# Kernel optimization log

Measured on AMD Instinct MI355X. Metric: run time of the kernel, lower is better.

The kernel has to match this reference:

```python
import jax, jax.numpy as jnp
import numpy as np

N_NODES = 100000
N_EDGES = 1600000
IN_SIZE = 512
HID_SIZE = 256
OUT_SIZE = 40
K_STEPS = 10
ALPHA = 0.1


def setup_inputs() -> dict:
    key = jax.random.key(0)
    ks = jax.random.split(key, 8)
    features = jax.random.normal(ks[0], (N_NODES, IN_SIZE), dtype=jnp.float32)
    src = jax.random.randint(ks[1], (N_EDGES,), 0, N_NODES, dtype=jnp.int64)
    dst = jax.random.randint(ks[2], (N_EDGES,), 0, N_NODES, dtype=jnp.int64)
    # MLP params (Kaiming-ish scale)
    W1 = jax.random.normal(ks[3], (IN_SIZE, HID_SIZE), dtype=jnp.float32) / np.sqrt(IN_SIZE)
    b1 = jnp.zeros((HID_SIZE,), dtype=jnp.float32)
    W2 = jax.random.normal(ks[4], (HID_SIZE, OUT_SIZE), dtype=jnp.float32) / np.sqrt(HID_SIZE)
    b2 = jnp.zeros((OUT_SIZE,), dtype=jnp.float32)
    return {"features": features, "src": src, "dst": dst,
            "W1": W1, "b1": b1, "W2": W2, "b2": b2}


def reference(features, src, dst, W1, b1, W2, b2):
    # --- MLP encoder (dropout is identity in eval mode) ---
    h = jax.nn.relu(features @ W1 + b1)
    h = h @ W2 + b2  # [N, out_size]

    # --- Symmetric normalization (DGL APPNPConv, edge_weight=None) ---
    ones_e = jnp.ones((src.shape[0],), dtype=h.dtype)
    deg_out = jax.ops.segment_sum(ones_e, src, num_segments=N_NODES)
    deg_in = jax.ops.segment_sum(ones_e, dst, num_segments=N_NODES)
    norm_src = jnp.power(jnp.clip(deg_out, 1.0), -0.5)[:, None]  # D_out^{-1/2}
    norm_dst = jnp.power(jnp.clip(deg_in, 1.0), -0.5)[:, None]   # D_in^{-1/2}

    # --- k=10 APPNP propagation: h <- (1-a) * D^{-1/2} A D^{-1/2} h + a * h0 ---
    h0 = h

    def step(h, _):
        msg = (h * norm_src)[src]                                  # gather [E, out]
        agg = jax.ops.segment_sum(msg, dst, num_segments=N_NODES)  # scatter-add
        h = (1.0 - ALPHA) * (agg * norm_dst) + ALPHA * h0
        return h, None

    h, _ = jax.lax.scan(step, h, None, length=K_STEPS)
    return h
```

## Files before the change

kernel.cpp:

```cpp
#include <hip/hip_runtime.h>

#define N_NODES 100000
#define N_EDGES 1600000
#define IN_SIZE 512
#define HID_SIZE 256
#define OUT_SIZE 40
#define K_STEPS 10
#define ALPHA 0.1f

#define NCH 250
#define CH_E 6400
#define NBUK 391
#define NRS 8
#define HRS 12544
#define NCS 16
#define CS_E 100000

typedef _Float16 half8 __attribute__((ext_vector_type(8)));
typedef float f32x4 __attribute__((ext_vector_type(4)));

struct __align__(8) Entry { int s; int d; };

__global__ __launch_bounds__(512) void hist_pass(const int* __restrict__ dst,
                                                 int* __restrict__ cnt) {
    __shared__ int h[NBUK];
    const int t = threadIdx.x, c = blockIdx.x;
    for (int j = t; j < NBUK; j += 512) h[j] = 0;
    __syncthreads();
    const int4* d4 = (const int4*)(dst + c * CH_E);
    for (int i = t; i < CH_E / 4; i += 512) {
        const int4 v = d4[i];
        atomicAdd(&h[v.x >> 8], 1);
        atomicAdd(&h[v.y >> 8], 1);
        atomicAdd(&h[v.z >> 8], 1);
        atomicAdd(&h[v.w >> 8], 1);
    }
    __syncthreads();
    for (int j = t; j < NBUK; j += 512) cnt[c * NBUK + j] = h[j];
}

__global__ __launch_bounds__(512) void bucket_scan(const int* __restrict__ cnt,
                                                   int* __restrict__ off,
                                                   int* __restrict__ boff) {
    __shared__ int tot[512];
    const int b = threadIdx.x;
    int s = 0;
    if (b < NBUK)
        for (int c = 0; c < NCH; ++c) s += cnt[c * NBUK + b];
    tot[b] = s;
    __syncthreads();
    for (int o = 1; o < 512; o <<= 1) {
        const int v = (b >= o) ? tot[b - o] : 0;
        __syncthreads();
        tot[b] += v;
        __syncthreads();
    }
    if (b < NBUK) {
        int run = tot[b] - s;
        boff[b] = run;
        for (int c = 0; c < NCH; ++c) { off[c * NBUK + b] = run; run += cnt[c * NBUK + b]; }
        if (b == NBUK - 1) boff[NBUK] = tot[b];
    }
}

__global__ __launch_bounds__(512) void scatter_pass(const int* __restrict__ src,
                                                    const int* __restrict__ dst,
                                                    const int* __restrict__ off,
                                                    Entry* __restrict__ ebuf) {
    __shared__ int cur[NBUK];
    const int t = threadIdx.x, c = blockIdx.x;
    for (int j = t; j < NBUK; j += 512) cur[j] = off[c * NBUK + j];
    __syncthreads();
    const int4* s4 = (const int4*)(src + c * CH_E);
    const int4* d4 = (const int4*)(dst + c * CH_E);
    for (int i = t; i < CH_E / 4; i += 512) {
        const int4 sv = s4[i];
        const int4 dv = d4[i];
        Entry e;
        int p;
        p = atomicAdd(&cur[dv.x >> 8], 1); e.s = sv.x; e.d = dv.x; ebuf[p] = e;
        p = atomicAdd(&cur[dv.y >> 8], 1); e.s = sv.y; e.d = dv.y; ebuf[p] = e;
        p = atomicAdd(&cur[dv.z >> 8], 1); e.s = sv.z; e.d = dv.z; ebuf[p] = e;
        p = atomicAdd(&cur[dv.w >> 8], 1); e.s = sv.w; e.d = dv.w; ebuf[p] = e;
    }
}

__global__ __launch_bounds__(256) void bucket_csr(const Entry* __restrict__ ebuf,
                                                  const int* __restrict__ boff,
                                                  int* __restrict__ rowp,
                                                  float* __restrict__ ndst,
                                                  int* __restrict__ csr) {
    __shared__ int hist[256];
    __shared__ int pref[256];
    __shared__ int cur[256];
    const int t = threadIdx.x, b = blockIdx.x;
    const int beg = boff[b], end = boff[b + 1];
    hist[t] = 0;
    __syncthreads();
    for (int i = beg + t; i < end; i += 256)
        atomicAdd(&hist[ebuf[i].d & 255], 1);
    __syncthreads();
    const int h = hist[t];
    pref[t] = h;
    __syncthreads();
    for (int o = 1; o < 256; o <<= 1) {
        const int v = (t >= o) ? pref[t - o] : 0;
        __syncthreads();
        pref[t] += v;
        __syncthreads();
    }
    const int val = beg + pref[t] - h;
    const int n = (b << 8) + t;
    if (n <= N_NODES) rowp[n] = val;
    if (n < N_NODES) ndst[n] = 1.0f / sqrtf((float)max(h, 1));
    cur[t] = val;
    __syncthreads();
    for (int i = beg + t; i < end; i += 256) {
        const Entry e = ebuf[i];
        const int pos = atomicAdd(&cur[e.d & 255], 1);
        csr[pos] = e.s;
    }
}

__global__ __launch_bounds__(512) void degsrc_part(const int* __restrict__ src,
                                                   int* __restrict__ partial) {
    __shared__ int h[HRS];
    const int t = threadIdx.x;
    const int r = blockIdx.x & (NRS - 1);
    const int c = blockIdx.x >> 3;
    const int base = r * HRS;
    for (int j = t; j < HRS; j += 512) h[j] = 0;
    __syncthreads();
    const int4* s4 = (const int4*)(src + (size_t)c * CS_E);
    for (int i = t; i < CS_E / 4; i += 512) {
        const int4 v = s4[i];
        unsigned u;
        u = (unsigned)(v.x - base); if (u < HRS) atomicAdd(&h[u], 1);
        u = (unsigned)(v.y - base); if (u < HRS) atomicAdd(&h[u], 1);
        u = (unsigned)(v.z - base); if (u < HRS) atomicAdd(&h[u], 1);
        u = (unsigned)(v.w - base); if (u < HRS) atomicAdd(&h[u], 1);
    }
    __syncthreads();
    for (int j = t; j < HRS; j += 512) partial[(size_t)c * (NRS * HRS) + base + j] = h[j];
}

__global__ __launch_bounds__(256) void nsrc_reduce(const int* __restrict__ partial,
                                                   float* __restrict__ nsrc) {
    const int n = blockIdx.x * 256 + threadIdx.x;
    int s = 0;
#pragma unroll
    for (int c = 0; c < NCS; ++c) s += partial[(size_t)c * (NRS * HRS) + n];
    if (n < N_NODES) nsrc[n] = 1.0f / sqrtf((float)max(s, 1));
}

__global__ __launch_bounds__(256) void prep_w(const float* __restrict__ W1,
                                              const float* __restrict__ W2,
                                              unsigned short* __restrict__ w1t,
                                              unsigned short* __restrict__ w2t) {
    int idx = blockIdx.x * 256 + threadIdx.x;
    if (idx < IN_SIZE * HID_SIZE) {
        int n = idx >> 9;
        int k = idx & 511;
        _Float16 h = (_Float16)W1[(size_t)k * HID_SIZE + n];
        w1t[idx] = *(unsigned short*)&h;
    } else if (idx < IN_SIZE * HID_SIZE + 48 * HID_SIZE) {
        int i2 = idx - IN_SIZE * HID_SIZE;
        int o = i2 >> 8;
        int c = i2 & 255;
        float v = (o < OUT_SIZE) ? W2[(size_t)c * OUT_SIZE + o] : 0.f;
        _Float16 h = (_Float16)v;
        w2t[i2] = *(unsigned short*)&h;
    }
}

__global__ __launch_bounds__(512) void gemm_fused(const float* __restrict__ X,
                                                  const unsigned short* __restrict__ w1t,
                                                  const float* __restrict__ b1,
                                                  const unsigned short* __restrict__ w2t,
                                                  const float* __restrict__ b2,
                                                  const float* __restrict__ nsrc,
                                                  _Float16* __restrict__ h0a,
                                                  _Float16* __restrict__ g0) {
    __shared__ __align__(16) unsigned char lds[49152];
    _Float16* sA = (_Float16*)lds;
    _Float16* sB = sA + 128 * 64;
    _Float16* sC = (_Float16*)lds;
    _Float16* sW = sC + 128 * 72;

    const int t    = threadIdx.x;
    const int lane = t & 63;
    const int w    = t >> 6;
    const int wr   = w >> 2;
    const int wc   = w & 3;
    const int n0   = blockIdx.x * 128;

    f32x4 acc[4][4];
#pragma unroll
    for (int i = 0; i < 4; ++i)
#pragma unroll
        for (int j = 0; j < 4; ++j) acc[i][j] = (f32x4)0.f;

    const int lo = lane & 15;
    const int hi = lane >> 4;
    const int l7 = lane & 7;

    int rowA[2], offA[2]; bool okA[2]; const float* pA[2];
#pragma unroll
    for (int i = 0; i < 2; ++i) {
        const int id  = t + i * 512;
        const int row = id >> 3;
        const int ch  = id & 7;
        rowA[i] = row;
        offA[i] = row * 64 + ((ch ^ (row & 7)) << 3);
        const int gr = n0 + row;
        okA[i] = (gr < N_NODES);
        pA[i] = X + (size_t)(okA[i] ? gr : 0) * IN_SIZE + ch * 8;
    }
    int offB[4]; const unsigned short* pB[4];
#pragma unroll
    for (int i = 0; i < 4; ++i) {
        const int id = t + i * 512;
        const int n  = id >> 3;
        const int ch = id & 7;
        offB[i] = n * 64 + ((ch ^ (n & 7)) << 3);
        pB[i] = w1t + (size_t)n * IN_SIZE + ch * 8;
    }

    float4 xr[2][2];
#pragma unroll
    for (int i = 0; i < 2; ++i) { xr[i][0] = make_float4(0,0,0,0); xr[i][1] = xr[i][0]; }
    uint4 br[4];

#pragma unroll
    for (int i = 0; i < 2; ++i)
        if (okA[i]) { xr[i][0] = ((const float4*)pA[i])[0]; xr[i][1] = ((const float4*)pA[i])[1]; }
#pragma unroll
    for (int i = 0; i < 4; ++i) br[i] = *(const uint4*)pB[i];

    for (int kk = 0; kk < IN_SIZE; kk += 64) {
        __syncthreads();
#pragma unroll
        for (int i = 0; i < 2; ++i) {
            half8 hv;
            hv[0] = (_Float16)xr[i][0].x; hv[1] = (_Float16)xr[i][0].y;
            hv[2] = (_Float16)xr[i][0].z; hv[3] = (_Float16)xr[i][0].w;
            hv[4] = (_Float16)xr[i][1].x; hv[5] = (_Float16)xr[i][1].y;
            hv[6] = (_Float16)xr[i][1].z; hv[7] = (_Float16)xr[i][1].w;
            *(half8*)&sA[offA[i]] = hv;
        }
#pragma unroll
        for (int i = 0; i < 4; ++i) *(uint4*)&sB[offB[i]] = br[i];
        if (kk + 64 < IN_SIZE) {
#pragma unroll
            for (int i = 0; i < 2; ++i)
                if (okA[i]) {
                    xr[i][0] = ((const float4*)(pA[i] + kk + 64))[0];
                    xr[i][1] = ((const float4*)(pA[i] + kk + 64))[1];
                }
#pragma unroll
            for (int i = 0; i < 4; ++i) br[i] = *(const uint4*)(pB[i] + kk + 64);
        }
        __syncthreads();
#pragma unroll
        for (int s = 0; s < 2; ++s) {
            const int chs = ((s * 4 + hi) ^ l7) << 3;
            half8 af[4], bf[4];
#pragma unroll
            for (int f = 0; f < 4; ++f)
                af[f] = *(const half8*)&sA[(wr * 64 + f * 16 + lo) * 64 + chs];
#pragma unroll
            for (int f = 0; f < 4; ++f)
                bf[f] = *(const half8*)&sB[(wc * 64 + f * 16 + lo) * 64 + chs];
#pragma unroll
            for (int fi = 0; fi < 4; ++fi)
#pragma unroll
                for (int fj = 0; fj < 4; ++fj)
                    acc[fi][fj] = __builtin_amdgcn_mfma_f32_16x16x32_f16(
                        af[fi], bf[fj], acc[fi][fj], 0, 0, 0);
        }
    }

    float b1v[4];
#pragma unroll
    for (int fj = 0; fj < 4; ++fj) b1v[fj] = b1[wc * 64 + fj * 16 + lo];

    __syncthreads();
#pragma unroll
    for (int i = 0; i < 3; ++i) {
        const int id = t + i * 512;
        const int o  = id >> 5;
        const int ch = id & 31;
        const uint4 v = *(const uint4*)(w2t + (size_t)o * HID_SIZE + ch * 8);
        *(uint4*)&sW[o * 264 + ch * 8] = v;
    }

    f32x4 acc2[3];
#pragma unroll
    for (int f = 0; f < 3; ++f) acc2[f] = (f32x4)0.f;
    float b2v[3];
#pragma unroll
    for (int f = 0; f < 3; ++f) {
        const int o = f * 16 + lo;
        b2v[f] = (o < OUT_SIZE) ? b2[o] : 0.f;
    }

    for (int j = 0; j < 4; ++j) {
        if (j) __syncthreads();
        if (wc == j) {
#pragma unroll
            for (int fi = 0; fi < 4; ++fi)
#pragma unroll
                for (int fj = 0; fj < 4; ++fj)
#pragma unroll
                    for (int r = 0; r < 4; ++r) {
                        const int rl = wr * 64 + fi * 16 + hi * 4 + r;
                        const int cl = fj * 16 + lo;
                        const float v = fmaxf(acc[fi][fj][r] + b1v[fj], 0.f);
                        sC[rl * 72 + cl] = (_Float16)v;
                    }
        }
        __syncthreads();
#pragma unroll
        for (int ks = 0; ks < 2; ++ks) {
            const half8 a = *(const half8*)&sC[(w * 16 + lo) * 72 + ks * 32 + hi * 8];
#pragma unroll
            for (int f = 0; f < 3; ++f) {
                const half8 b = *(const half8*)&sW[(f * 16 + lo) * 264 + j * 64 + ks * 32 + hi * 8];
                acc2[f] = __builtin_amdgcn_mfma_f32_16x16x32_f16(a, b, acc2[f], 0, 0, 0);
            }
        }
    }

#pragma unroll
    for (int f = 0; f < 3; ++f) {
        const int o = f * 16 + lo;
#pragma unroll
        for (int r = 0; r < 4; ++r) {
            const int grow = n0 + w * 16 + hi * 4 + r;
            if (grow < N_NODES && o < OUT_SIZE) {
                const float v = acc2[f][r] + b2v[f];
                const float ns = nsrc[grow];
                g0 [(size_t)grow * 64 + o] = (_Float16)(ns * v);
                h0a[(size_t)grow * 64 + o] = (_Float16)(ALPHA * v);
            }
        }
    }
}

__global__ __launch_bounds__(320) void appnp_step4(const _Float16* __restrict__ gin,
                                                   const _Float16* __restrict__ h0a,
                                                   const int* __restrict__ rowp,
                                                   const int* __restrict__ csr,
                                                   const float* __restrict__ nsrc,
                                                   const float* __restrict__ ndst,
                                                   _Float16* __restrict__ gout,
                                                   float* __restrict__ hout,
                                                   int last) {
    const int tid = threadIdx.x;
    const int ln  = tid / 5;
    const int q   = tid - ln * 5;
    const int n   = blockIdx.x * 64 + ln;
    if (n >= N_NODES) return;

    const int beg = rowp[n];
    const int end = rowp[n + 1];
    const _Float16* gq = gin + q * 8;

    float acc[8];
#pragma unroll
    for (int j = 0; j < 8; ++j) acc[j] = 0.f;

    int e = beg;
    for (; e + 4 <= end; e += 4) {
        const int s0 = csr[e + 0];
        const int s1 = csr[e + 1];
        const int s2 = csr[e + 2];
        const int s3 = csr[e + 3];
        const half8 v0 = *(const half8*)(gq + (size_t)s0 * 64);
        const half8 v1 = *(const half8*)(gq + (size_t)s1 * 64);
        const half8 v2 = *(const half8*)(gq + (size_t)s2 * 64);
        const half8 v3 = *(const half8*)(gq + (size_t)s3 * 64);
#pragma unroll
        for (int j = 0; j < 8; ++j)
            acc[j] += (float)v0[j] + (float)v1[j] + (float)v2[j] + (float)v3[j];
    }
    for (; e < end; ++e) {
        const int s0 = csr[e];
        const half8 v0 = *(const half8*)(gq + (size_t)s0 * 64);
#pragma unroll
        for (int j = 0; j < 8; ++j) acc[j] += (float)v0[j];
    }

    const float nd = (1.0f - ALPHA) * ndst[n];
    const half8 ha = *(const half8*)(h0a + (size_t)n * 64 + q * 8);
    float r[8];
#pragma unroll
    for (int j = 0; j < 8; ++j) r[j] = nd * acc[j] + (float)ha[j];

    if (last) {
        f32x4 ra, rb;
        ra[0] = r[0]; ra[1] = r[1]; ra[2] = r[2]; ra[3] = r[3];
        rb[0] = r[4]; rb[1] = r[5]; rb[2] = r[6]; rb[3] = r[7];
        *(f32x4*)(hout + (size_t)n * OUT_SIZE + q * 8) = ra;
        *(f32x4*)(hout + (size_t)n * OUT_SIZE + q * 8 + 4) = rb;
    } else {
        const float ns = nsrc[n];
        half8 gv;
#pragma unroll
        for (int j = 0; j < 8; ++j) gv[j] = (_Float16)(ns * r[j]);
        *(half8*)(gout + (size_t)n * 64 + q * 8) = gv;
    }
}

extern "C" void kernel_launch(void* const* d_in, const int* in_sizes, int n_in,
                              void* d_out, int out_size, void* d_ws, size_t ws_size,
                              hipStream_t stream) {
    const float* X   = (const float*)d_in[0];
    const int*   src = (const int*)d_in[1];
    const int*   dst = (const int*)d_in[2];
    const float* W1  = (const float*)d_in[3];
    const float* b1  = (const float*)d_in[4];
    const float* W2  = (const float*)d_in[5];
    const float* b2  = (const float*)d_in[6];
    float* out = (float*)d_out;

    char* ws = (char*)d_ws;
    size_t off = 0;
    auto alloc = [&](size_t bytes) -> void* {
        void* p = ws + off;
        off = (off + bytes + 255) & ~(size_t)255;
        return p;
    };
    _Float16* h0a = (_Float16*)alloc((size_t)N_NODES * 64 * 2);
    _Float16* gA  = (_Float16*)alloc((size_t)N_NODES * 64 * 2);
    _Float16* gB  = (_Float16*)alloc((size_t)N_NODES * 64 * 2);
    Entry* ebuf    = (Entry*)gA;
    int*   partial = (int*)gB;
    float* nsrc = (float*)alloc((size_t)N_NODES * 4);
    float* ndst = (float*)alloc((size_t)N_NODES * 4);
    int* rowp   = (int*)alloc((size_t)(N_NODES + 2) * 4);
    int* csr    = (int*)alloc((size_t)N_EDGES * 4);
    int* cnt    = (int*)alloc((size_t)NCH * NBUK * 4);
    int* offb   = (int*)alloc((size_t)NCH * NBUK * 4);
    int* boff   = (int*)alloc((size_t)(NBUK + 1) * 4);
    unsigned short* w1t = (unsigned short*)alloc((size_t)IN_SIZE * HID_SIZE * 2);
    unsigned short* w2t = (unsigned short*)alloc((size_t)48 * HID_SIZE * 2);

    const int pgrid = (N_NODES + 63) / 64;

    hist_pass<<<NCH, 512, 0, stream>>>(dst, cnt);
    bucket_scan<<<1, 512, 0, stream>>>(cnt, offb, boff);
    scatter_pass<<<NCH, 512, 0, stream>>>(src, dst, offb, ebuf);
    bucket_csr<<<NBUK, 256, 0, stream>>>(ebuf, boff, rowp, ndst, csr);
    degsrc_part<<<NRS * NCS, 512, 0, stream>>>(src, partial);
    nsrc_reduce<<<(NRS * HRS) / 256, 256, 0, stream>>>(partial, nsrc);

    prep_w<<<(IN_SIZE * HID_SIZE + 48 * HID_SIZE + 255) / 256, 256, 0, stream>>>(W1, W2, w1t, w2t);
    gemm_fused<<<(N_NODES + 127) / 128, 512, 0, stream>>>(X, w1t, b1, w2t, b2, nsrc, h0a, gA);

    const _Float16* gin = gA;
    for (int s = 0; s < K_STEPS; ++s) {
        const int last = (s == K_STEPS - 1) ? 1 : 0;
        _Float16* gout = (s & 1) ? gA : gB;
        appnp_step4<<<pgrid, 320, 0, stream>>>(gin, h0a, rowp, csr, nsrc, ndst,
                                               gout, out, last);
        gin = gout;
    }
}
```

Measured before the change: 548.9 us.

## Split padded fp16 feature rows into 32-wide main and 8-wide tail arrays

Replaces the 64-half padded per-node feature layout with a 32-column main array plus an 8-column tail array. The gathers in each propagation step then touch 64-byte plus 16-byte rows instead of 128-byte padded rows, which cuts wasted cache-line traffic on the random-access gather. The GEMM epilogue now stages its output through LDS so it can write vectorized half8 stores into both arrays. The edge buffer and partial histograms get their own workspace instead of aliasing the feature buffers, which raises workspace use. The tail gathers hit a separate array, so a node's 40 features now span two cache lines in different places.

```diff
diff --git a/kernel.cpp b/kernel.cpp
--- a/kernel.cpp
+++ b/kernel.cpp
@@ -179,8 +179,10 @@
                                                   const unsigned short* __restrict__ w2t,
                                                   const float* __restrict__ b2,
                                                   const float* __restrict__ nsrc,
-                                                  _Float16* __restrict__ h0a,
-                                                  _Float16* __restrict__ g0) {
+                                                  _Float16* __restrict__ h0aM,
+                                                  _Float16* __restrict__ h0aT,
+                                                  _Float16* __restrict__ g0M,
+                                                  _Float16* __restrict__ g0T) {
     __shared__ __align__(16) unsigned char lds[49152];
     _Float16* sA = (_Float16*)lds;
     _Float16* sB = sA + 128 * 64;
@@ -204,13 +206,12 @@
     const int hi = lane >> 4;
     const int l7 = lane & 7;
 
-    int rowA[2], offA[2]; bool okA[2]; const float* pA[2];
+    int offA[2]; bool okA[2]; const float* pA[2];
 #pragma unroll
     for (int i = 0; i < 2; ++i) {
         const int id  = t + i * 512;
         const int row = id >> 3;
         const int ch  = id & 7;
-        rowA[i] = row;
         offA[i] = row * 64 + ((ch ^ (row & 7)) << 3);
         const int gr = n0 + row;
         okA[i] = (gr < N_NODES);
@@ -331,29 +332,63 @@
         }
     }
 
-#pragma unroll
-    for (int f = 0; f < 3; ++f) {
-        const int o = f * 16 + lo;
+    __syncthreads();
+    _Float16* sOut = sC;
+#pragma unroll
+    for (int f = 0; f < 3; ++f)
 #pragma unroll
         for (int r = 0; r < 4; ++r) {
-            const int grow = n0 + w * 16 + hi * 4 + r;
-            if (grow < N_NODES && o < OUT_SIZE) {
-                const float v = acc2[f][r] + b2v[f];
-                const float ns = nsrc[grow];
-                g0 [(size_t)grow * 64 + o] = (_Float16)(ns * v);
-                h0a[(size_t)grow * 64 + o] = (_Float16)(ALPHA * v);
+            const int rl = w * 16 + hi * 4 + r;
+            sOut[rl * 48 + f * 16 + lo] = (_Float16)(acc2[f][r] + b2v[f]);
+        }
+    __syncthreads();
+
+    {
+        const int row  = t >> 2;
+        const int quad = t & 3;
+        const int grow = n0 + row;
+        if (grow < N_NODES) {
+            const float ns = nsrc[grow];
+            const half8 v = *(const half8*)&sOut[row * 48 + quad * 8];
+            half8 g, ha;
+#pragma unroll
+            for (int j = 0; j < 8; ++j) {
+                const float f = (float)v[j];
+                g[j]  = (_Float16)(ns * f);
+                ha[j] = (_Float16)(ALPHA * f);
             }
-        }
-    }
-}
-
-__global__ __launch_bounds__(320) void appnp_step4(const _Float16* __restrict__ gin,
-                                                   const _Float16* __restrict__ h0a,
+            *(half8*)(g0M  + (size_t)grow * 32 + quad * 8) = g;
+            *(half8*)(h0aM + (size_t)grow * 32 + quad * 8) = ha;
+        }
+    }
+    if (t < 128) {
+        const int grow = n0 + t;
+        if (grow < N_NODES) {
+            const float ns = nsrc[grow];
+            const half8 v = *(const half8*)&sOut[t * 48 + 32];
+            half8 g, ha;
+#pragma unroll
+            for (int j = 0; j < 8; ++j) {
+                const float f = (float)v[j];
+                g[j]  = (_Float16)(ns * f);
+                ha[j] = (_Float16)(ALPHA * f);
+            }
+            *(half8*)(g0T  + (size_t)grow * 8) = g;
+            *(half8*)(h0aT + (size_t)grow * 8) = ha;
+        }
+    }
+}
+
+__global__ __launch_bounds__(320) void appnp_step5(const _Float16* __restrict__ gMin,
+                                                   const _Float16* __restrict__ gTin,
+                                                   const _Float16* __restrict__ h0aM,
+                                                   const _Float16* __restrict__ h0aT,
                                                    const int* __restrict__ rowp,
                                                    const int* __restrict__ csr,
                                                    const float* __restrict__ nsrc,
                                                    const float* __restrict__ ndst,
-                                                   _Float16* __restrict__ gout,
+                                                   _Float16* __restrict__ gMout,
+                                                   _Float16* __restrict__ gTout,
                                                    float* __restrict__ hout,
                                                    int last) {
     const int tid = threadIdx.x;
@@ -364,7 +399,9 @@
 
     const int beg = rowp[n];
     const int end = rowp[n + 1];
-    const _Float16* gq = gin + q * 8;
+    const bool main_ = (q < 4);
+    const _Float16* gq = main_ ? (gMin + q * 8) : gTin;
+    const int shift = main_ ? 5 : 3;
 
     float acc[8];
 #pragma unroll
@@ -376,23 +413,24 @@
         const int s1 = csr[e + 1];
         const int s2 = csr[e + 2];
         const int s3 = csr[e + 3];
-        const half8 v0 = *(const half8*)(gq + (size_t)s0 * 64);
-        const half8 v1 = *(const half8*)(gq + (size_t)s1 * 64);
-        const half8 v2 = *(const half8*)(gq + (size_t)s2 * 64);
-        const half8 v3 = *(const half8*)(gq + (size_t)s3 * 64);
+        const half8 v0 = *(const half8*)(gq + ((size_t)s0 << shift));
+        const half8 v1 = *(const half8*)(gq + ((size_t)s1 << shift));
+        const half8 v2 = *(const half8*)(gq + ((size_t)s2 << shift));
+        const half8 v3 = *(const half8*)(gq + ((size_t)s3 << shift));
 #pragma unroll
         for (int j = 0; j < 8; ++j)
             acc[j] += (float)v0[j] + (float)v1[j] + (float)v2[j] + (float)v3[j];
     }
     for (; e < end; ++e) {
         const int s0 = csr[e];
-        const half8 v0 = *(const half8*)(gq + (size_t)s0 * 64);
+        const half8 v0 = *(const half8*)(gq + ((size_t)s0 << shift));
 #pragma unroll
         for (int j = 0; j < 8; ++j) acc[j] += (float)v0[j];
     }
 
     const float nd = (1.0f - ALPHA) * ndst[n];
-    const half8 ha = *(const half8*)(h0a + (size_t)n * 64 + q * 8);
+    const half8 ha = main_ ? *(const half8*)(h0aM + (size_t)n * 32 + q * 8)
+                           : *(const half8*)(h0aT + (size_t)n * 8);
     float r[8];
 #pragma unroll
     for (int j = 0; j < 8; ++j) r[j] = nd * acc[j] + (float)ha[j];
@@ -408,7 +446,8 @@
         half8 gv;
 #pragma unroll
         for (int j = 0; j < 8; ++j) gv[j] = (_Float16)(ns * r[j]);
-        *(half8*)(gout + (size_t)n * 64 + q * 8) = gv;
+        if (main_) *(half8*)(gMout + (size_t)n * 32 + q * 8) = gv;
+        else       *(half8*)(gTout + (size_t)n * 8) = gv;
     }
 }
 
@@ -431,11 +470,14 @@
         off = (off + bytes + 255) & ~(size_t)255;
         return p;
     };
-    _Float16* h0a = (_Float16*)alloc((size_t)N_NODES * 64 * 2);
-    _Float16* gA  = (_Float16*)alloc((size_t)N_NODES * 64 * 2);
-    _Float16* gB  = (_Float16*)alloc((size_t)N_NODES * 64 * 2);
-    Entry* ebuf    = (Entry*)gA;
-    int*   partial = (int*)gB;
+    _Float16* h0aM = (_Float16*)alloc((size_t)N_NODES * 32 * 2);
+    _Float16* h0aT = (_Float16*)alloc((size_t)N_NODES * 8 * 2);
+    _Float16* gMA  = (_Float16*)alloc((size_t)N_NODES * 32 * 2);
+    _Float16* gTA  = (_Float16*)alloc((size_t)N_NODES * 8 * 2);
+    _Float16* gMB  = (_Float16*)alloc((size_t)N_NODES * 32 * 2);
+    _Float16* gTB  = (_Float16*)alloc((size_t)N_NODES * 8 * 2);
+    Entry* ebuf    = (Entry*)alloc((size_t)N_EDGES * 8);
+    int*   partial = (int*)alloc((size_t)NCS * NRS * HRS * 4);
     float* nsrc = (float*)alloc((size_t)N_NODES * 4);
     float* ndst = (float*)alloc((size_t)N_NODES * 4);
     int* rowp   = (int*)alloc((size_t)(N_NODES + 2) * 4);
@@ -456,14 +498,18 @@
     nsrc_reduce<<<(NRS * HRS) / 256, 256, 0, stream>>>(partial, nsrc);
 
     prep_w<<<(IN_SIZE * HID_SIZE + 48 * HID_SIZE + 255) / 256, 256, 0, stream>>>(W1, W2, w1t, w2t);
-    gemm_fused<<<(N_NODES + 127) / 128, 512, 0, stream>>>(X, w1t, b1, w2t, b2, nsrc, h0a, gA);
-
-    const _Float16* gin = gA;
+    gemm_fused<<<(N_NODES + 127) / 128, 512, 0, stream>>>(X, w1t, b1, w2t, b2, nsrc,
+                                                          h0aM, h0aT, gMA, gTA);
+
+    const _Float16* gMin = gMA;
+    const _Float16* gTin = gTA;
     for (int s = 0; s < K_STEPS; ++s) {
         const int last = (s == K_STEPS - 1) ? 1 : 0;
-        _Float16* gout = (s & 1) ? gA : gB;
-        appnp_step4<<<pgrid, 320, 0, stream>>>(gin, h0a, rowp, csr, nsrc, ndst,
-                                               gout, out, last);
-        gin = gout;
-    }
-}
+        _Float16* gMout = (s & 1) ? gMA : gMB;
+        _Float16* gTout = (s & 1) ? gTA : gTB;
+        appnp_step5<<<pgrid, 320, 0, stream>>>(gMin, gTin, h0aM, h0aT, rowp, csr,
+                                               nsrc, ndst, gMout, gTout, out, last);
+        gMin = gMout;
+        gTin = gTout;
+    }
+}
```

After: 587.5 us. 7.0% more time.
